# Optimization experiments

Hardware: AMD Instinct MI355X
Metric: run time of the kernel (lower is better)

Reference implementation:

```python
import jax, jax.numpy as jnp
import numpy as np

B, K, D = 64, 2048, 32400  # batch, num bases, in_features**2 (180*180)


def setup_inputs() -> dict:
    key = jax.random.key(0)
    k1, k2, k3, k4, k5, k6 = jax.random.split(key, 6)
    s = 1.0 / np.sqrt(K)  # matches uniform(-sqrt(1/K), sqrt(1/K)) scale of weight init
    return {
        "X_re": jax.random.normal(k1, (B, D), dtype=jnp.float32),
        "X_im": jax.random.normal(k2, (B, D), dtype=jnp.float32),
        "bases_re": jax.random.normal(k3, (K, D), dtype=jnp.float32) * 0.004,
        "bases_im": jax.random.normal(k4, (K, D), dtype=jnp.float32) * 0.004,
        "weight_re": jax.random.normal(k5, (K,), dtype=jnp.float32) * s,
        "weight_im": jax.random.normal(k6, (K,), dtype=jnp.float32) * s,
    }


def reference(X_re, X_im, bases_re, bases_im, weight_re, weight_im):
    # Assemble complex64 operands
    X = jax.lax.complex(X_re, X_im)          # [B, D]
    bases = jax.lax.complex(bases_re, bases_im)  # [K, D]
    w = jax.lax.complex(weight_re, weight_im)    # [K]
    # X @ conj(bases)^T -> [B, K]; diag_embed(weight) matmul == per-basis scale
    coeffs = jnp.matmul(X, jnp.conj(bases).T) * w[None, :]
    # project back: [B, K] @ [K, D] -> [B, D]
    out = jnp.matmul(coeffs, bases)
    # complex->channels->complex round trip in the original is the identity
    return out
```

## Files before the change

kernel.cpp:

```cpp
#include <hip/hip_runtime.h>
#include <hip/hip_bf16.h>
#include <cstdint>
#include <cstddef>

#define B_DIM 64
#define K_DIM 2048
#define D_DIM 32400
#define KTILE 128

typedef __bf16 bf16x8 __attribute__((ext_vector_type(8)));
typedef float f32x4 __attribute__((ext_vector_type(4)));

union U128 { uint4 u; bf16x8 b; };

__device__ inline bf16x8 asbf(uint4 u) { U128 x; x.u = u; return x.b; }

__device__ inline uint4 neg4(uint4 u) {
    u.x ^= 0x80008000u; u.y ^= 0x80008000u; u.z ^= 0x80008000u; u.w ^= 0x80008000u;
    return u;
}

__device__ inline f32x4 mfma16(bf16x8 a, bf16x8 b, f32x4 c) {
    return __builtin_amdgcn_mfma_f32_16x16x32_bf16(a, b, c, 0, 0, 0);
}

__device__ inline f32x4 ld4g(const float* __restrict__ p, int d, int dlim) {
    f32x4 r;
    if (d + 4 <= dlim) {
        float4 v = *reinterpret_cast<const float4*>(p + d);
        r[0] = v.x; r[1] = v.y; r[2] = v.z; r[3] = v.w;
    } else {
        #pragma unroll
        for (int j = 0; j < 4; ++j) r[j] = (d + j < dlim) ? p[d + j] : 0.0f;
    }
    return r;
}

__device__ inline uint4 ld8bf(const __bf16* __restrict__ p, int d, int dlim) {
    if (d + 8 <= dlim) return *reinterpret_cast<const uint4*>(p + d);
    union { uint4 u; __bf16 h[8]; } x;
    #pragma unroll
    for (int j = 0; j < 8; ++j) x.h[j] = (d + j < dlim) ? p[d + j] : (__bf16)0.0f;
    return x.u;
}

__device__ inline uint32_t pk(float a, float b) {
    union { __bf16 h[2]; uint32_t u; } x;
    x.h[0] = (__bf16)a; x.h[1] = (__bf16)b;
    return x.u;
}

__global__ __launch_bounds__(256) void xbf_kernel(
    const float* __restrict__ Xre, const float* __restrict__ Xim,
    __bf16* __restrict__ XreB, __bf16* __restrict__ XimB)
{
    const int i = (blockIdx.x * 256 + threadIdx.x) * 4;
    if (i < B_DIM * D_DIM) {
        float4 a = *reinterpret_cast<const float4*>(Xre + i);
        float4 b = *reinterpret_cast<const float4*>(Xim + i);
        *(uint2*)(XreB + i) = make_uint2(pk(a.x, a.y), pk(a.z, a.w));
        *(uint2*)(XimB + i) = make_uint2(pk(b.x, b.y), pk(b.z, b.w));
    }
}

#define P1_STRIDE 72

template <bool XBF>
__global__ __launch_bounds__(256, 2) void p1_coeffs(
    const float* __restrict__ XreF, const float* __restrict__ XimF,
    const __bf16* __restrict__ XreB, const __bf16* __restrict__ XimB,
    const float* __restrict__ Bre, const float* __restrict__ Bim,
    const float* __restrict__ Wre, const float* __restrict__ Wim,
    float* __restrict__ Cre, float* __restrict__ Cim)
{
    __shared__ __align__(16) __bf16 sX[2][64][P1_STRIDE];
    __shared__ __align__(16) __bf16 sB[2][KTILE][P1_STRIDE];

    const int ktg = blockIdx.x;
    const int dc  = blockIdx.y;
    const int tid  = threadIdx.x;
    const int lane = tid & 63;
    const int w    = tid >> 6;
    const int r    = lane & 15;
    const int g    = lane >> 4;

    const int kbase  = ktg * KTILE;
    const int dstart = dc * 1024;
    const int dend   = min(dstart + 1024, D_DIM);
    const int nsteps = (dend - dstart + 63) >> 6;

    const int srow = tid >> 4;
    const int sd   = (tid & 15) * 4;
    const int rowx = tid >> 3;
    const int colx = (tid & 7) * 8;

    f32x4 bst[16];
    uint4 xst[4];
    f32x4 xstf[8];

    auto LOADS = [&](int s) {
        const int dg = dstart + s * 64 + sd;
        #pragma unroll
        for (int j = 0; j < 8; ++j) {
            const int row = j * 16 + srow;
            bst[j]     = ld4g(Bre + (size_t)(kbase + row) * D_DIM, dg, dend);
            bst[8 + j] = ld4g(Bim + (size_t)(kbase + row) * D_DIM, dg, dend);
        }
        if (XBF) {
            const int dgx = dstart + s * 64 + colx;
            xst[0] = ld8bf(XreB + (size_t)rowx * D_DIM,        dgx, dend);
            xst[1] = ld8bf(XreB + (size_t)(rowx + 32) * D_DIM, dgx, dend);
            xst[2] = ld8bf(XimB + (size_t)rowx * D_DIM,        dgx, dend);
            xst[3] = ld8bf(XimB + (size_t)(rowx + 32) * D_DIM, dgx, dend);
        } else {
            #pragma unroll
            for (int j = 0; j < 4; ++j) {
                const int row = j * 16 + srow;
                xstf[j]     = ld4g(XreF + (size_t)row * D_DIM, dg, dend);
                xstf[4 + j] = ld4g(XimF + (size_t)row * D_DIM, dg, dend);
            }
        }
    };

    auto WRITE = [&]() {
        #pragma unroll
        for (int j = 0; j < 8; ++j) {
            const int row = j * 16 + srow;
            *(uint2*)&sB[0][row][sd] = make_uint2(pk(bst[j][0],     bst[j][1]),     pk(bst[j][2],     bst[j][3]));
            *(uint2*)&sB[1][row][sd] = make_uint2(pk(bst[8 + j][0], bst[8 + j][1]), pk(bst[8 + j][2], bst[8 + j][3]));
        }
        if (XBF) {
            *(uint4*)&sX[0][rowx][colx]      = xst[0];
            *(uint4*)&sX[0][rowx + 32][colx] = xst[1];
            *(uint4*)&sX[1][rowx][colx]      = xst[2];
            *(uint4*)&sX[1][rowx + 32][colx] = xst[3];
        } else {
            #pragma unroll
            for (int j = 0; j < 4; ++j) {
                const int row = j * 16 + srow;
                *(uint2*)&sX[0][row][sd] = make_uint2(pk(xstf[j][0],     xstf[j][1]),     pk(xstf[j][2],     xstf[j][3]));
                *(uint2*)&sX[1][row][sd] = make_uint2(pk(xstf[4 + j][0], xstf[4 + j][1]), pk(xstf[4 + j][2], xstf[4 + j][3]));
            }
        }
    };

    const int m0  = (w & 1) * 32;
    const int nl0 = (w >> 1) * 64;

    f32x4 accRe[2][4] = {};
    f32x4 accIm[2][4] = {};

    auto COMPUTE = [&]() {
        #pragma unroll
        for (int kk = 0; kk < 2; ++kk) {
            const int dp = kk * 32 + g * 8;
            uint4 xre[2], xim[2], bre[4], bim[4];
            #pragma unroll
            for (int ms = 0; ms < 2; ++ms) {
                xre[ms] = *(const uint4*)&sX[0][m0 + ms * 16 + r][dp];
                xim[ms] = *(const uint4*)&sX[1][m0 + ms * 16 + r][dp];
            }
            #pragma unroll
            for (int ns = 0; ns < 4; ++ns) {
                bre[ns] = *(const uint4*)&sB[0][nl0 + ns * 16 + r][dp];
                bim[ns] = *(const uint4*)&sB[1][nl0 + ns * 16 + r][dp];
            }
            #pragma unroll
            for (int ms = 0; ms < 2; ++ms)
            #pragma unroll
            for (int ns = 0; ns < 4; ++ns) {
                accRe[ms][ns] = mfma16(asbf(xre[ms]), asbf(bre[ns]), accRe[ms][ns]);
                accRe[ms][ns] = mfma16(asbf(xim[ms]), asbf(bim[ns]), accRe[ms][ns]);
                accIm[ms][ns] = mfma16(asbf(xim[ms]), asbf(bre[ns]), accIm[ms][ns]);
                accIm[ms][ns] = mfma16(asbf(neg4(xre[ms])), asbf(bim[ns]), accIm[ms][ns]);
            }
        }
    };

    LOADS(0); WRITE(); __syncthreads();
    for (int s = 0; s < nsteps; ++s) {
        if (s + 1 < nsteps) LOADS(s + 1);
        COMPUTE();
        if (s + 1 < nsteps) {
            __syncthreads();
            WRITE();
            __syncthreads();
        }
    }

    #pragma unroll
    for (int ms = 0; ms < 2; ++ms)
    #pragma unroll
    for (int ns = 0; ns < 4; ++ns) {
        const int kb = kbase + nl0 + ns * 16 + r;
        const float wre = Wre[kb], wim = Wim[kb];
        #pragma unroll
        for (int i = 0; i < 4; ++i) {
            const int b = m0 + ms * 16 + g * 4 + i;
            const float cre = accRe[ms][ns][i];
            const float cim = accIm[ms][ns][i];
            atomicAdd(&Cre[b * K_DIM + kb], cre * wre - cim * wim);
            atomicAdd(&Cim[b * K_DIM + kb], cre * wim + cim * wre);
        }
    }
}

__global__ __launch_bounds__(256) void cbf_kernel(
    const float* __restrict__ Cre, const float* __restrict__ Cim,
    __bf16* __restrict__ CreBf, __bf16* __restrict__ CimBf)
{
    const int i = blockIdx.x * 256 + threadIdx.x;
    if (i < B_DIM * K_DIM) {
        CreBf[i] = (__bf16)Cre[i];
        CimBf[i] = (__bf16)Cim[i];
    }
}

#define P2_STRIDE 72

template <bool WIM>
__global__ __launch_bounds__(256) void p2_project(
    const float* __restrict__ Bre, const float* __restrict__ Bim,
    const __bf16* __restrict__ CreBf, const __bf16* __restrict__ CimBf,
    float* __restrict__ out)
{
    __shared__ __align__(16) __bf16 sT[2][2][64][P2_STRIDE];

    const int dt = blockIdx.x;
    const int kh = blockIdx.y;
    const int d0 = dt * 64;
    const int khbase = kh * (K_DIM / 2);
    const int tid  = threadIdx.x;
    const int lane = tid & 63;
    const int w    = tid >> 6;
    const int r    = lane & 15;
    const int g    = lane >> 4;

    const int kq = tid >> 4;
    const int ds = (tid & 15) * 4;

    f32x4 st[8];

    auto LOADS = [&](int t) {
        const int k0 = khbase + t * 64;
        #pragma unroll
        for (int j = 0; j < 4; ++j) {
            const size_t ro = (size_t)(k0 + kq * 4 + j) * D_DIM;
            st[j]     = ld4g(Bre + ro, d0 + ds, D_DIM);
            st[4 + j] = ld4g(Bim + ro, d0 + ds, D_DIM);
        }
    };

    auto WRITE = [&](int buf) {
        #pragma unroll
        for (int i = 0; i < 4; ++i) {
            *(uint2*)&sT[buf][0][ds + i][kq * 4] =
                make_uint2(pk(st[0][i], st[1][i]), pk(st[2][i], st[3][i]));
            *(uint2*)&sT[buf][1][ds + i][kq * 4] =
                make_uint2(pk(st[4][i], st[5][i]), pk(st[6][i], st[7][i]));
        }
    };

    const int m0  = (w & 1) * 32;
    const int nl0 = (w >> 1) * 32;

    f32x4 accRe[2][2] = {};
    f32x4 accIm[2][2] = {};

    auto COMPUTE = [&](int t, int buf) {
        const int k0 = khbase + t * 64;
        uint4 aRe[2][2], aIm[2][2];
        #pragma unroll
        for (int ms = 0; ms < 2; ++ms) {
            const size_t rowo = (size_t)(m0 + ms * 16 + r) * K_DIM;
            #pragma unroll
            for (int kk = 0; kk < 2; ++kk) {
                aRe[ms][kk] = *(const uint4*)&CreBf[rowo + k0 + kk * 32 + g * 8];
                aIm[ms][kk] = *(const uint4*)&CimBf[rowo + k0 + kk * 32 + g * 8];
            }
        }
        #pragma unroll
        for (int kk = 0; kk < 2; ++kk) {
            uint4 bre[2], bim[2];
            #pragma unroll
            for (int ns = 0; ns < 2; ++ns) {
                bre[ns] = *(const uint4*)&sT[buf][0][nl0 + ns * 16 + r][kk * 32 + g * 8];
                bim[ns] = *(const uint4*)&sT[buf][1][nl0 + ns * 16 + r][kk * 32 + g * 8];
            }
            #pragma unroll
            for (int ms = 0; ms < 2; ++ms)
            #pragma unroll
            for (int ns = 0; ns < 2; ++ns) {
                accRe[ms][ns] = mfma16(asbf(aRe[ms][kk]), asbf(bre[ns]), accRe[ms][ns]);
                accRe[ms][ns] = mfma16(asbf(neg4(aIm[ms][kk])), asbf(bim[ns]), accRe[ms][ns]);
                if (WIM) {
                    accIm[ms][ns] = mfma16(asbf(aRe[ms][kk]), asbf(bim[ns]), accIm[ms][ns]);
                    accIm[ms][ns] = mfma16(asbf(aIm[ms][kk]), asbf(bre[ns]), accIm[ms][ns]);
                }
            }
        }
    };

    const int NT = (K_DIM / 2) / 64;
    LOADS(0); WRITE(0); __syncthreads();
    for (int t = 0; t < NT; ++t) {
        if (t + 1 < NT) LOADS(t + 1);
        COMPUTE(t, t & 1);
        if (t + 1 < NT) WRITE((t + 1) & 1);
        __syncthreads();
    }

    #pragma unroll
    for (int ms = 0; ms < 2; ++ms)
    #pragma unroll
    for (int ns = 0; ns < 2; ++ns) {
        const int d = d0 + nl0 + ns * 16 + r;
        if (d < D_DIM) {
            #pragma unroll
            for (int i = 0; i < 4; ++i) {
                const int b = m0 + ms * 16 + g * 4 + i;
                if (!WIM) {
                    atomicAdd(&out[(size_t)b * D_DIM + d], accRe[ms][ns][i]);
                } else {
                    atomicAdd(&out[((size_t)b * D_DIM + d) * 2],     accRe[ms][ns][i]);
                    atomicAdd(&out[((size_t)b * D_DIM + d) * 2 + 1], accIm[ms][ns][i]);
                }
            }
        }
    }
}

extern "C" void kernel_launch(void* const* d_in, const int* in_sizes, int n_in,
                              void* d_out, int out_size, void* d_ws, size_t ws_size,
                              hipStream_t stream) {
    const float* Xre = (const float*)d_in[0];
    const float* Xim = (const float*)d_in[1];
    const float* Bre = (const float*)d_in[2];
    const float* Bim = (const float*)d_in[3];
    const float* Wre = (const float*)d_in[4];
    const float* Wim = (const float*)d_in[5];

    float*  Cre   = (float*)d_ws;
    float*  Cim   = Cre + B_DIM * K_DIM;
    __bf16* CreBf = (__bf16*)(Cim + B_DIM * K_DIM);
    __bf16* CimBf = CreBf + B_DIM * K_DIM;
    __bf16* XreB  = CimBf + B_DIM * K_DIM;
    __bf16* XimB  = XreB + (size_t)B_DIM * D_DIM;

    const size_t need = (size_t)2 * B_DIM * K_DIM * sizeof(float)
                      + (size_t)2 * B_DIM * K_DIM * sizeof(__bf16)
                      + (size_t)2 * B_DIM * D_DIM * sizeof(__bf16);
    const bool xbf = ws_size >= need;

    (void)hipMemsetAsync(d_ws, 0, (size_t)2 * B_DIM * K_DIM * sizeof(float), stream);
    (void)hipMemsetAsync(d_out, 0, (size_t)out_size * sizeof(float), stream);

    dim3 g1(K_DIM / KTILE, 32);
    if (xbf) {
        xbf_kernel<<<(B_DIM * D_DIM / 4 + 255) / 256, 256, 0, stream>>>(Xre, Xim, XreB, XimB);
        p1_coeffs<true><<<g1, 256, 0, stream>>>(Xre, Xim, XreB, XimB, Bre, Bim, Wre, Wim, Cre, Cim);
    } else {
        p1_coeffs<false><<<g1, 256, 0, stream>>>(Xre, Xim, XreB, XimB, Bre, Bim, Wre, Wim, Cre, Cim);
    }

    cbf_kernel<<<(B_DIM * K_DIM + 255) / 256, 256, 0, stream>>>(Cre, Cim, CreBf, CimBf);

    const int ndt = (D_DIM + 63) / 64;
    dim3 g2(ndt, 2);
    if (out_size == 2 * B_DIM * D_DIM) {
        p2_project<true><<<g2, 256, 0, stream>>>(Bre, Bim, CreBf, CimBf, (float*)d_out);
    } else {
        p2_project<false><<<g2, 256, 0, stream>>>(Bre, Bim, CreBf, CimBf, (float*)d_out);
    }
}
```

Before: 304.1 us.

## Stream X directly from global, widen D step, and swizzle bases LDS

The coefficient kernel stops staging X through shared memory. Each wave now loads its X fragments straight from global memory (bf16, or fp32 packed on the fly) inside the compute loop. The D step per iteration doubles from 64 to 128, and the bases tile uses an XOR-swizzled unpadded layout to avoid bank conflicts. Bases are converted to bf16 at load time, which shrinks staging registers. The cost is that X loads now sit on the compute critical path with no prefetch, and each X element is fetched by two waves that previously shared it through LDS.

```diff
diff --git a/kernel.cpp b/kernel.cpp
--- a/kernel.cpp
+++ b/kernel.cpp
@@ -7,6 +7,7 @@
 #define K_DIM 2048
 #define D_DIM 32400
 #define KTILE 128
+#define KS    128
 
 typedef __bf16 bf16x8 __attribute__((ext_vector_type(8)));
 typedef float f32x4 __attribute__((ext_vector_type(4)));
@@ -63,8 +64,6 @@
     }
 }
 
-#define P1_STRIDE 72
-
 template <bool XBF>
 __global__ __launch_bounds__(256, 2) void p1_coeffs(
     const float* __restrict__ XreF, const float* __restrict__ XimF,
@@ -73,8 +72,7 @@
     const float* __restrict__ Wre, const float* __restrict__ Wim,
     float* __restrict__ Cre, float* __restrict__ Cim)
 {
-    __shared__ __align__(16) __bf16 sX[2][64][P1_STRIDE];
-    __shared__ __align__(16) __bf16 sB[2][KTILE][P1_STRIDE];
+    __shared__ __align__(16) __bf16 sB[2][KTILE][KS];
 
     const int ktg = blockIdx.x;
     const int dc  = blockIdx.y;
@@ -87,60 +85,38 @@
     const int kbase  = ktg * KTILE;
     const int dstart = dc * 1024;
     const int dend   = min(dstart + 1024, D_DIM);
-    const int nsteps = (dend - dstart + 63) >> 6;
-
-    const int srow = tid >> 4;
-    const int sd   = (tid & 15) * 4;
-    const int rowx = tid >> 3;
-    const int colx = (tid & 7) * 8;
-
-    f32x4 bst[16];
-    uint4 xst[4];
-    f32x4 xstf[8];
+    const int nsteps = (dend - dstart + KS - 1) / KS;
+
+    const int srow = tid >> 5;
+    const int sdx  = (tid & 31) * 4;
+
+    uint2 stb[32];
 
     auto LOADS = [&](int s) {
-        const int dg = dstart + s * 64 + sd;
-        #pragma unroll
-        for (int j = 0; j < 8; ++j) {
-            const int row = j * 16 + srow;
-            bst[j]     = ld4g(Bre + (size_t)(kbase + row) * D_DIM, dg, dend);
-            bst[8 + j] = ld4g(Bim + (size_t)(kbase + row) * D_DIM, dg, dend);
-        }
-        if (XBF) {
-            const int dgx = dstart + s * 64 + colx;
-            xst[0] = ld8bf(XreB + (size_t)rowx * D_DIM,        dgx, dend);
-            xst[1] = ld8bf(XreB + (size_t)(rowx + 32) * D_DIM, dgx, dend);
-            xst[2] = ld8bf(XimB + (size_t)rowx * D_DIM,        dgx, dend);
-            xst[3] = ld8bf(XimB + (size_t)(rowx + 32) * D_DIM, dgx, dend);
-        } else {
-            #pragma unroll
-            for (int j = 0; j < 4; ++j) {
-                const int row = j * 16 + srow;
-                xstf[j]     = ld4g(XreF + (size_t)row * D_DIM, dg, dend);
-                xstf[4 + j] = ld4g(XimF + (size_t)row * D_DIM, dg, dend);
-            }
-        }
+        const int dg = dstart + s * KS + sdx;
+        #pragma unroll
+        for (int j = 0; j < 16; ++j) {
+            const int row = j * 8 + srow;
+            f32x4 a = ld4g(Bre + (size_t)(kbase + row) * D_DIM, dg, dend);
+            f32x4 b = ld4g(Bim + (size_t)(kbase + row) * D_DIM, dg, dend);
+            stb[j]      = make_uint2(pk(a[0], a[1]), pk(a[2], a[3]));
+            stb[16 + j] = make_uint2(pk(b[0], b[1]), pk(b[2], b[3]));
+        }
+    };
+
+    auto lds_off = [&](int row, int delem) -> uint32_t {
+        return ((uint32_t)(row * (KS * 2) + delem * 2)) ^ (uint32_t)((row & 7) << 4);
     };
 
     auto WRITE = [&]() {
-        #pragma unroll
-        for (int j = 0; j < 8; ++j) {
-            const int row = j * 16 + srow;
-            *(uint2*)&sB[0][row][sd] = make_uint2(pk(bst[j][0],     bst[j][1]),     pk(bst[j][2],     bst[j][3]));
-            *(uint2*)&sB[1][row][sd] = make_uint2(pk(bst[8 + j][0], bst[8 + j][1]), pk(bst[8 + j][2], bst[8 + j][3]));
-        }
-        if (XBF) {
-            *(uint4*)&sX[0][rowx][colx]      = xst[0];
-            *(uint4*)&sX[0][rowx + 32][colx] = xst[1];
-            *(uint4*)&sX[1][rowx][colx]      = xst[2];
-            *(uint4*)&sX[1][rowx + 32][colx] = xst[3];
-        } else {
-            #pragma unroll
-            for (int j = 0; j < 4; ++j) {
-                const int row = j * 16 + srow;
-                *(uint2*)&sX[0][row][sd] = make_uint2(pk(xstf[j][0],     xstf[j][1]),     pk(xstf[j][2],     xstf[j][3]));
-                *(uint2*)&sX[1][row][sd] = make_uint2(pk(xstf[4 + j][0], xstf[4 + j][1]), pk(xstf[4 + j][2], xstf[4 + j][3]));
-            }
+        char* b0 = (char*)&sB[0][0][0];
+        char* b1 = (char*)&sB[1][0][0];
+        #pragma unroll
+        for (int j = 0; j < 16; ++j) {
+            const int row = j * 8 + srow;
+            const uint32_t off = lds_off(row, sdx);
+            *(uint2*)(b0 + off) = stb[j];
+            *(uint2*)(b1 + off) = stb[16 + j];
         }
     };
 
@@ -150,20 +126,32 @@
     f32x4 accRe[2][4] = {};
     f32x4 accIm[2][4] = {};
 
-    auto COMPUTE = [&]() {
-        #pragma unroll
-        for (int kk = 0; kk < 2; ++kk) {
-            const int dp = kk * 32 + g * 8;
+    auto COMPUTE = [&](int s) {
+        const char* b0 = (const char*)&sB[0][0][0];
+        const char* b1 = (const char*)&sB[1][0][0];
+        #pragma unroll
+        for (int kk = 0; kk < 4; ++kk) {
+            const int del = kk * 32 + g * 8;
+            const int dg  = dstart + s * KS + del;
             uint4 xre[2], xim[2], bre[4], bim[4];
             #pragma unroll
             for (int ms = 0; ms < 2; ++ms) {
-                xre[ms] = *(const uint4*)&sX[0][m0 + ms * 16 + r][dp];
-                xim[ms] = *(const uint4*)&sX[1][m0 + ms * 16 + r][dp];
+                const size_t xo = (size_t)(m0 + ms * 16 + r) * D_DIM;
+                if (XBF) {
+                    xre[ms] = ld8bf(XreB + xo, dg, dend);
+                    xim[ms] = ld8bf(XimB + xo, dg, dend);
+                } else {
+                    f32x4 a0 = ld4g(XreF + xo, dg, dend), a1 = ld4g(XreF + xo, dg + 4, dend);
+                    f32x4 c0 = ld4g(XimF + xo, dg, dend), c1 = ld4g(XimF + xo, dg + 4, dend);
+                    xre[ms] = make_uint4(pk(a0[0], a0[1]), pk(a0[2], a0[3]), pk(a1[0], a1[1]), pk(a1[2], a1[3]));
+                    xim[ms] = make_uint4(pk(c0[0], c0[1]), pk(c0[2], c0[3]), pk(c1[0], c1[1]), pk(c1[2], c1[3]));
+                }
             }
             #pragma unroll
             for (int ns = 0; ns < 4; ++ns) {
-                bre[ns] = *(const uint4*)&sB[0][nl0 + ns * 16 + r][dp];
-                bim[ns] = *(const uint4*)&sB[1][nl0 + ns * 16 + r][dp];
+                const uint32_t off = lds_off(nl0 + ns * 16 + r, del);
+                bre[ns] = *(const uint4*)(b0 + off);
+                bim[ns] = *(const uint4*)(b1 + off);
             }
             #pragma unroll
             for (int ms = 0; ms < 2; ++ms)
@@ -180,7 +168,7 @@
     LOADS(0); WRITE(); __syncthreads();
     for (int s = 0; s < nsteps; ++s) {
         if (s + 1 < nsteps) LOADS(s + 1);
-        COMPUTE();
+        COMPUTE(s);
         if (s + 1 < nsteps) {
             __syncthreads();
             WRITE();
```

Result: slower. 390.2 us (+28.3%).

## Cache bf16 tiled copy of bases in pass 1 for reuse in projection

Applied to the files above, without the earlier changes.

Pass 1 now writes the bf16-converted bases into a workspace buffer laid out as 64-column d tiles. Pass 2 reads this compact bf16 copy instead of re-reading and converting the fp32 bases. This halves the bytes pass 2 reads but adds a large write stream to pass 1, and it needs a big workspace. Total memory traffic stays roughly the same.

```diff
diff --git a/kernel.cpp b/kernel.cpp
--- a/kernel.cpp
+++ b/kernel.cpp
@@ -7,6 +7,7 @@
 #define K_DIM 2048
 #define D_DIM 32400
 #define KTILE 128
+#define NDT   507
 
 typedef __bf16 bf16x8 __attribute__((ext_vector_type(8)));
 typedef float f32x4 __attribute__((ext_vector_type(4)));
@@ -65,12 +66,13 @@
 
 #define P1_STRIDE 72
 
-template <bool XBF>
+template <bool XBF, bool WB>
 __global__ __launch_bounds__(256, 2) void p1_coeffs(
     const float* __restrict__ XreF, const float* __restrict__ XimF,
     const __bf16* __restrict__ XreB, const __bf16* __restrict__ XimB,
     const float* __restrict__ Bre, const float* __restrict__ Bim,
     const float* __restrict__ Wre, const float* __restrict__ Wim,
+    __bf16* __restrict__ BTre, __bf16* __restrict__ BTim,
     float* __restrict__ Cre, float* __restrict__ Cim)
 {
     __shared__ __align__(16) __bf16 sX[2][64][P1_STRIDE];
@@ -94,17 +96,25 @@
     const int rowx = tid >> 3;
     const int colx = (tid & 7) * 8;
 
-    f32x4 bst[16];
+    uint2 pRe[8], pIm[8];
     uint4 xst[4];
     f32x4 xstf[8];
 
     auto LOADS = [&](int s) {
         const int dg = dstart + s * 64 + sd;
+        const int dt = dc * 16 + s;
         #pragma unroll
         for (int j = 0; j < 8; ++j) {
             const int row = j * 16 + srow;
-            bst[j]     = ld4g(Bre + (size_t)(kbase + row) * D_DIM, dg, dend);
-            bst[8 + j] = ld4g(Bim + (size_t)(kbase + row) * D_DIM, dg, dend);
+            f32x4 a = ld4g(Bre + (size_t)(kbase + row) * D_DIM, dg, dend);
+            f32x4 b = ld4g(Bim + (size_t)(kbase + row) * D_DIM, dg, dend);
+            pRe[j] = make_uint2(pk(a[0], a[1]), pk(a[2], a[3]));
+            pIm[j] = make_uint2(pk(b[0], b[1]), pk(b[2], b[3]));
+            if (WB) {
+                const size_t bo = ((size_t)dt * K_DIM + (kbase + row)) * 64 + sd;
+                *(uint2*)&BTre[bo] = pRe[j];
+                *(uint2*)&BTim[bo] = pIm[j];
+            }
         }
         if (XBF) {
             const int dgx = dstart + s * 64 + colx;
@@ -126,8 +136,8 @@
         #pragma unroll
         for (int j = 0; j < 8; ++j) {
             const int row = j * 16 + srow;
-            *(uint2*)&sB[0][row][sd] = make_uint2(pk(bst[j][0],     bst[j][1]),     pk(bst[j][2],     bst[j][3]));
-            *(uint2*)&sB[1][row][sd] = make_uint2(pk(bst[8 + j][0], bst[8 + j][1]), pk(bst[8 + j][2], bst[8 + j][3]));
+            *(uint2*)&sB[0][row][sd] = pRe[j];
+            *(uint2*)&sB[1][row][sd] = pIm[j];
         }
         if (XBF) {
             *(uint4*)&sX[0][rowx][colx]      = xst[0];
@@ -218,9 +228,10 @@
 
 #define P2_STRIDE 72
 
-template <bool WIM>
+template <bool WIM, bool BTP>
 __global__ __launch_bounds__(256) void p2_project(
     const float* __restrict__ Bre, const float* __restrict__ Bim,
+    const __bf16* __restrict__ BTre, const __bf16* __restrict__ BTim,
     const __bf16* __restrict__ CreBf, const __bf16* __restrict__ CimBf,
     float* __restrict__ out)
 {
@@ -240,24 +251,49 @@
     const int ds = (tid & 15) * 4;
 
     f32x4 st[8];
+    uint2 su[8];
 
     auto LOADS = [&](int t) {
         const int k0 = khbase + t * 64;
-        #pragma unroll
-        for (int j = 0; j < 4; ++j) {
-            const size_t ro = (size_t)(k0 + kq * 4 + j) * D_DIM;
-            st[j]     = ld4g(Bre + ro, d0 + ds, D_DIM);
-            st[4 + j] = ld4g(Bim + ro, d0 + ds, D_DIM);
+        if (BTP) {
+            #pragma unroll
+            for (int j = 0; j < 4; ++j) {
+                const size_t bo = ((size_t)dt * K_DIM + (k0 + kq * 4 + j)) * 64 + ds;
+                su[j]     = *(const uint2*)&BTre[bo];
+                su[4 + j] = *(const uint2*)&BTim[bo];
+            }
+        } else {
+            #pragma unroll
+            for (int j = 0; j < 4; ++j) {
+                const size_t ro = (size_t)(k0 + kq * 4 + j) * D_DIM;
+                st[j]     = ld4g(Bre + ro, d0 + ds, D_DIM);
+                st[4 + j] = ld4g(Bim + ro, d0 + ds, D_DIM);
+            }
         }
     };
 
     auto WRITE = [&](int buf) {
-        #pragma unroll
-        for (int i = 0; i < 4; ++i) {
-            *(uint2*)&sT[buf][0][ds + i][kq * 4] =
-                make_uint2(pk(st[0][i], st[1][i]), pk(st[2][i], st[3][i]));
-            *(uint2*)&sT[buf][1][ds + i][kq * 4] =
-                make_uint2(pk(st[4][i], st[5][i]), pk(st[6][i], st[7][i]));
+        if (BTP) {
+            union { uint2 u; ushort h[4]; } re[4], im[4];
+            #pragma unroll
+            for (int j = 0; j < 4; ++j) { re[j].u = su[j]; im[j].u = su[4 + j]; }
+            #pragma unroll
+            for (int i = 0; i < 4; ++i) {
+                *(uint2*)&sT[buf][0][ds + i][kq * 4] = make_uint2(
+                    (uint32_t)re[0].h[i] | ((uint32_t)re[1].h[i] << 16),
+                    (uint32_t)re[2].h[i] | ((uint32_t)re[3].h[i] << 16));
+                *(uint2*)&sT[buf][1][ds + i][kq * 4] = make_uint2(
+                    (uint32_t)im[0].h[i] | ((uint32_t)im[1].h[i] << 16),
+                    (uint32_t)im[2].h[i] | ((uint32_t)im[3].h[i] << 16));
+            }
+        } else {
+            #pragma unroll
+            for (int i = 0; i < 4; ++i) {
+                *(uint2*)&sT[buf][0][ds + i][kq * 4] =
+                    make_uint2(pk(st[0][i], st[1][i]), pk(st[2][i], st[3][i]));
+                *(uint2*)&sT[buf][1][ds + i][kq * 4] =
+                    make_uint2(pk(st[4][i], st[5][i]), pk(st[6][i], st[7][i]));
+            }
         }
     };
 
@@ -346,11 +382,15 @@
     __bf16* CimBf = CreBf + B_DIM * K_DIM;
     __bf16* XreB  = CimBf + B_DIM * K_DIM;
     __bf16* XimB  = XreB + (size_t)B_DIM * D_DIM;
-
-    const size_t need = (size_t)2 * B_DIM * K_DIM * sizeof(float)
-                      + (size_t)2 * B_DIM * K_DIM * sizeof(__bf16)
-                      + (size_t)2 * B_DIM * D_DIM * sizeof(__bf16);
-    const bool xbf = ws_size >= need;
+    __bf16* BTre  = XimB + (size_t)B_DIM * D_DIM;
+    __bf16* BTim  = BTre + (size_t)NDT * K_DIM * 64;
+
+    const size_t needX = (size_t)2 * B_DIM * K_DIM * sizeof(float)
+                       + (size_t)2 * B_DIM * K_DIM * sizeof(__bf16)
+                       + (size_t)2 * B_DIM * D_DIM * sizeof(__bf16);
+    const size_t needBT = needX + (size_t)2 * NDT * K_DIM * 64 * sizeof(__bf16);
+    const bool xbf = ws_size >= needX;
+    const bool bt  = ws_size >= needBT;
 
     (void)hipMemsetAsync(d_ws, 0, (size_t)2 * B_DIM * K_DIM * sizeof(float), stream);
     (void)hipMemsetAsync(d_out, 0, (size_t)out_size * sizeof(float), stream);
@@ -358,18 +398,21 @@
     dim3 g1(K_DIM / KTILE, 32);
     if (xbf) {
         xbf_kernel<<<(B_DIM * D_DIM / 4 + 255) / 256, 256, 0, stream>>>(Xre, Xim, XreB, XimB);
-        p1_coeffs<true><<<g1, 256, 0, stream>>>(Xre, Xim, XreB, XimB, Bre, Bim, Wre, Wim, Cre, Cim);
+        if (bt) p1_coeffs<true, true><<<g1, 256, 0, stream>>>(Xre, Xim, XreB, XimB, Bre, Bim, Wre, Wim, BTre, BTim, Cre, Cim);
+        else    p1_coeffs<true, false><<<g1, 256, 0, stream>>>(Xre, Xim, XreB, XimB, Bre, Bim, Wre, Wim, BTre, BTim, Cre, Cim);
     } else {
-        p1_coeffs<false><<<g1, 256, 0, stream>>>(Xre, Xim, XreB, XimB, Bre, Bim, Wre, Wim, Cre, Cim);
+        p1_coeffs<false, false><<<g1, 256, 0, stream>>>(Xre, Xim, XreB, XimB, Bre, Bim, Wre, Wim, BTre, BTim, Cre, Cim);
     }
 
     cbf_kernel<<<(B_DIM * K_DIM + 255) / 256, 256, 0, stream>>>(Cre, Cim, CreBf, CimBf);
 
-    const int ndt = (D_DIM + 63) / 64;
-    dim3 g2(ndt, 2);
-    if (out_size == 2 * B_DIM * D_DIM) {
-        p2_project<true><<<g2, 256, 0, stream>>>(Bre, Bim, CreBf, CimBf, (float*)d_out);
+    dim3 g2(NDT, 2);
+    const bool wim = (out_size == 2 * B_DIM * D_DIM);
+    if (wim) {
+        if (bt) p2_project<true, true><<<g2, 256, 0, stream>>>(Bre, Bim, BTre, BTim, CreBf, CimBf, (float*)d_out);
+        else    p2_project<true, false><<<g2, 256, 0, stream>>>(Bre, Bim, BTre, BTim, CreBf, CimBf, (float*)d_out);
     } else {
-        p2_project<false><<<g2, 256, 0, stream>>>(Bre, Bim, CreBf, CimBf, (float*)d_out);
-    }
-}
+        if (bt) p2_project<false, true><<<g2, 256, 0, stream>>>(Bre, Bim, BTre, BTim, CreBf, CimBf, (float*)d_out);
+        else    p2_project<false, false><<<g2, 256, 0, stream>>>(Bre, Bim, BTre, BTim, CreBf, CimBf, (float*)d_out);
+    }
+}
```

New measurement: 396.4 us. 30.3% more time.

## Swizzle p1 shared tiles, single-buffer p2 and raise occupancy bounds

Applied to the files above, without the earlier changes.

In the coefficient kernel, the padded shared-memory layout (stride 72) becomes an unpadded 128-byte-row layout with an XOR swizzle. This shrinks LDS use while keeping bank conflicts low, so the launch-bounds occupancy hint rises from 2 to 3 blocks. In the projection kernel, the double-buffered LDS tile becomes a single buffer with an extra barrier before each write, and the launch bounds request 5 blocks per CU. The cost is an extra sync per step in p2 and possible register pressure or spills from the tighter bounds.

```diff
diff --git a/kernel.cpp b/kernel.cpp
--- a/kernel.cpp
+++ b/kernel.cpp
@@ -63,18 +63,20 @@
     }
 }
 
-#define P1_STRIDE 72
+__device__ inline int swz128(int row, int delem) {
+    return (row * 128 + delem * 2) ^ ((row & 7) << 4);
+}
 
 template <bool XBF>
-__global__ __launch_bounds__(256, 2) void p1_coeffs(
+__global__ __launch_bounds__(256, 3) void p1_coeffs(
     const float* __restrict__ XreF, const float* __restrict__ XimF,
     const __bf16* __restrict__ XreB, const __bf16* __restrict__ XimB,
     const float* __restrict__ Bre, const float* __restrict__ Bim,
     const float* __restrict__ Wre, const float* __restrict__ Wim,
     float* __restrict__ Cre, float* __restrict__ Cim)
 {
-    __shared__ __align__(16) __bf16 sX[2][64][P1_STRIDE];
-    __shared__ __align__(16) __bf16 sB[2][KTILE][P1_STRIDE];
+    __shared__ __align__(16) __bf16 sX[2][64 * 64];
+    __shared__ __align__(16) __bf16 sB[2][KTILE * 64];
 
     const int ktg = blockIdx.x;
     const int dc  = blockIdx.y;
@@ -123,23 +125,29 @@
     };
 
     auto WRITE = [&]() {
+        char* b0 = (char*)&sB[0][0];
+        char* b1 = (char*)&sB[1][0];
         #pragma unroll
         for (int j = 0; j < 8; ++j) {
             const int row = j * 16 + srow;
-            *(uint2*)&sB[0][row][sd] = make_uint2(pk(bst[j][0],     bst[j][1]),     pk(bst[j][2],     bst[j][3]));
-            *(uint2*)&sB[1][row][sd] = make_uint2(pk(bst[8 + j][0], bst[8 + j][1]), pk(bst[8 + j][2], bst[8 + j][3]));
-        }
+            const int off = swz128(row, sd);
+            *(uint2*)(b0 + off) = make_uint2(pk(bst[j][0],     bst[j][1]),     pk(bst[j][2],     bst[j][3]));
+            *(uint2*)(b1 + off) = make_uint2(pk(bst[8 + j][0], bst[8 + j][1]), pk(bst[8 + j][2], bst[8 + j][3]));
+        }
+        char* x0 = (char*)&sX[0][0];
+        char* x1 = (char*)&sX[1][0];
         if (XBF) {
-            *(uint4*)&sX[0][rowx][colx]      = xst[0];
-            *(uint4*)&sX[0][rowx + 32][colx] = xst[1];
-            *(uint4*)&sX[1][rowx][colx]      = xst[2];
-            *(uint4*)&sX[1][rowx + 32][colx] = xst[3];
+            *(uint4*)(x0 + swz128(rowx, colx))      = xst[0];
+            *(uint4*)(x0 + swz128(rowx + 32, colx)) = xst[1];
+            *(uint4*)(x1 + swz128(rowx, colx))      = xst[2];
+            *(uint4*)(x1 + swz128(rowx + 32, colx)) = xst[3];
         } else {
             #pragma unroll
             for (int j = 0; j < 4; ++j) {
                 const int row = j * 16 + srow;
-                *(uint2*)&sX[0][row][sd] = make_uint2(pk(xstf[j][0],     xstf[j][1]),     pk(xstf[j][2],     xstf[j][3]));
-                *(uint2*)&sX[1][row][sd] = make_uint2(pk(xstf[4 + j][0], xstf[4 + j][1]), pk(xstf[4 + j][2], xstf[4 + j][3]));
+                const int off = swz128(row, sd);
+                *(uint2*)(x0 + off) = make_uint2(pk(xstf[j][0],     xstf[j][1]),     pk(xstf[j][2],     xstf[j][3]));
+                *(uint2*)(x1 + off) = make_uint2(pk(xstf[4 + j][0], xstf[4 + j][1]), pk(xstf[4 + j][2], xstf[4 + j][3]));
             }
         }
     };
@@ -151,19 +159,25 @@
     f32x4 accIm[2][4] = {};
 
     auto COMPUTE = [&]() {
+        const char* x0 = (const char*)&sX[0][0];
+        const char* x1 = (const char*)&sX[1][0];
+        const char* b0 = (const char*)&sB[0][0];
+        const char* b1 = (const char*)&sB[1][0];
         #pragma unroll
         for (int kk = 0; kk < 2; ++kk) {
             const int dp = kk * 32 + g * 8;
             uint4 xre[2], xim[2], bre[4], bim[4];
             #pragma unroll
             for (int ms = 0; ms < 2; ++ms) {
-                xre[ms] = *(const uint4*)&sX[0][m0 + ms * 16 + r][dp];
-                xim[ms] = *(const uint4*)&sX[1][m0 + ms * 16 + r][dp];
+                const int off = swz128(m0 + ms * 16 + r, dp);
+                xre[ms] = *(const uint4*)(x0 + off);
+                xim[ms] = *(const uint4*)(x1 + off);
             }
             #pragma unroll
             for (int ns = 0; ns < 4; ++ns) {
-                bre[ns] = *(const uint4*)&sB[0][nl0 + ns * 16 + r][dp];
-                bim[ns] = *(const uint4*)&sB[1][nl0 + ns * 16 + r][dp];
+                const int off = swz128(nl0 + ns * 16 + r, dp);
+                bre[ns] = *(const uint4*)(b0 + off);
+                bim[ns] = *(const uint4*)(b1 + off);
             }
             #pragma unroll
             for (int ms = 0; ms < 2; ++ms)
@@ -219,12 +233,12 @@
 #define P2_STRIDE 72
 
 template <bool WIM>
-__global__ __launch_bounds__(256) void p2_project(
+__global__ __launch_bounds__(256, 5) void p2_project(
     const float* __restrict__ Bre, const float* __restrict__ Bim,
     const __bf16* __restrict__ CreBf, const __bf16* __restrict__ CimBf,
     float* __restrict__ out)
 {
-    __shared__ __align__(16) __bf16 sT[2][2][64][P2_STRIDE];
+    __shared__ __align__(16) __bf16 sT[2][64][P2_STRIDE];
 
     const int dt = blockIdx.x;
     const int kh = blockIdx.y;
@@ -251,12 +265,12 @@
         }
     };
 
-    auto WRITE = [&](int buf) {
+    auto WRITE = [&]() {
         #pragma unroll
         for (int i = 0; i < 4; ++i) {
-            *(uint2*)&sT[buf][0][ds + i][kq * 4] =
+            *(uint2*)&sT[0][ds + i][kq * 4] =
                 make_uint2(pk(st[0][i], st[1][i]), pk(st[2][i], st[3][i]));
-            *(uint2*)&sT[buf][1][ds + i][kq * 4] =
+            *(uint2*)&sT[1][ds + i][kq * 4] =
                 make_uint2(pk(st[4][i], st[5][i]), pk(st[6][i], st[7][i]));
         }
     };
@@ -267,7 +281,7 @@
     f32x4 accRe[2][2] = {};
     f32x4 accIm[2][2] = {};
 
-    auto COMPUTE = [&](int t, int buf) {
+    auto COMPUTE = [&](int t) {
         const int k0 = khbase + t * 64;
         uint4 aRe[2][2], aIm[2][2];
         #pragma unroll
@@ -284,8 +298,8 @@
             uint4 bre[2], bim[2];
             #pragma unroll
             for (int ns = 0; ns < 2; ++ns) {
-                bre[ns] = *(const uint4*)&sT[buf][0][nl0 + ns * 16 + r][kk * 32 + g * 8];
-                bim[ns] = *(const uint4*)&sT[buf][1][nl0 + ns * 16 + r][kk * 32 + g * 8];
+                bre[ns] = *(const uint4*)&sT[0][nl0 + ns * 16 + r][kk * 32 + g * 8];
+                bim[ns] = *(const uint4*)&sT[1][nl0 + ns * 16 + r][kk * 32 + g * 8];
             }
             #pragma unroll
             for (int ms = 0; ms < 2; ++ms)
@@ -302,12 +316,15 @@
     };
 
     const int NT = (K_DIM / 2) / 64;
-    LOADS(0); WRITE(0); __syncthreads();
+    LOADS(0); WRITE(); __syncthreads();
     for (int t = 0; t < NT; ++t) {
         if (t + 1 < NT) LOADS(t + 1);
-        COMPUTE(t, t & 1);
-        if (t + 1 < NT) WRITE((t + 1) & 1);
-        __syncthreads();
+        COMPUTE(t);
+        if (t + 1 < NT) {
+            __syncthreads();
+            WRITE();
+            __syncthreads();
+        }
     }
 
     #pragma unroll
```

Measured after the change: 646.1 us. +112.4%, slower.
